# Kernel optimization log

Measured on AMD Instinct MI355X. Metric: run time of the kernel, lower is better.

Reference implementation:

```python
import jax, jax.numpy as jnp
import numpy as np

T, B, V, D, H, C = 2048, 32, 50257, 512, 768, 10


def setup_inputs() -> dict:
    key = jax.random.key(0)
    ks = jax.random.split(key, 11)
    s = 0.02
    return {
        "x": jax.random.randint(ks[0], (T, B), 0, V),
        "embed_table": jax.random.normal(ks[1], (V, D), jnp.float32) * s,
        "W_x": jax.random.normal(ks[2], (H, D), jnp.float32) * s,
        "W_f": jax.random.normal(ks[3], (H, D), jnp.float32) * s,
        "b_f": jax.random.normal(ks[4], (H,), jnp.float32) * s,
        "W_r": jax.random.normal(ks[5], (H, D), jnp.float32) * s,
        "b_r": jax.random.normal(ks[6], (H,), jnp.float32) * s,
        "W_cx": jax.random.normal(ks[7], (H, D), jnp.float32) * s,
        "b_cx": jax.random.normal(ks[8], (H,), jnp.float32) * s,
        "W_out": jax.random.normal(ks[9], (C, H), jnp.float32) * s,
        "b_out": jax.random.normal(ks[10], (C,), jnp.float32) * s,
    }


def reference(x, embed_table, W_x, W_f, b_f, W_r, b_r, W_cx, b_cx, W_out, b_out):
    # Embedding lookup: [T, B, D]
    e = embed_table[x]
    # Precompute all gate projections for every timestep (batched GEMMs).
    xp = jnp.einsum("tbd,hd->tbh", e, W_x)                 # x_t projection
    f = jax.nn.sigmoid(jnp.einsum("tbd,hd->tbh", e, W_f) + b_f)   # forget gate
    r = jax.nn.sigmoid(jnp.einsum("tbd,hd->tbh", e, W_r) + b_r)   # reset gate
    cx = jnp.einsum("tbd,hd->tbh", e, W_cx) + b_cx                # highway path

    c0 = jnp.zeros((B, H), e.dtype)  # init_hidden: zeros

    def step(c, inp):
        f_t, xp_t, r_t, cx_t = inp
        c = f_t * c + (1.0 - f_t) * xp_t
        h = r_t * jnp.tanh(c) + (1.0 - r_t) * cx_t
        return c, h

    _, ht = jax.lax.scan(step, c0, (f, xp, r, cx))  # ht: [T, B, H]

    # tanh -> max-pool over time -> tanh -> classifier
    pooled = jnp.max(jnp.tanh(ht), axis=0)          # [B, H]
    pooled = jnp.tanh(pooled)
    logit = pooled @ W_out.T + b_out                # [B, C]
    return logit
```

## Files before the change

kernel.cpp:

```cpp
#include <hip/hip_runtime.h>
#include <hip/hip_bf16.h>
#include <cstdint>
#include <cstddef>

#define T_DIM 2048
#define B_DIM 32
#define D_DIM 512
#define H_DIM 768
#define C_DIM 10
#define K_DIM D_DIM
#define N_DIM (4 * H_DIM)

#define TC 1024
#define NCHUNK (T_DIM / TC)
#define MC (TC * B_DIM)

#define L_SEG 64
#define S_SEG (TC / L_SEG)
#define BH (B_DIM * H_DIM)

typedef __attribute__((ext_vector_type(8))) short short8;
typedef __attribute__((ext_vector_type(4))) float float4v;

__device__ inline unsigned short f2bf(float f) {
  unsigned int u = __builtin_bit_cast(unsigned int, f);
  unsigned int r = (u + 0x7FFFu + ((u >> 16) & 1u)) >> 16;
  return (unsigned short)r;
}
__device__ inline float bf2f(unsigned short s) {
  unsigned int u = ((unsigned int)s) << 16;
  return __builtin_bit_cast(float, u);
}
__device__ inline float fast_rcp(float x) { return __builtin_amdgcn_rcpf(x); }
__device__ inline float fast_exp2(float x) { return __builtin_amdgcn_exp2f(x); }
__device__ inline float sigmoid_f(float x) {
  float e = fast_exp2(-1.4426950408889634f * x);
  return fast_rcp(1.0f + e);
}
__device__ inline float tanh_f(float x) {
  float e = fast_exp2(2.885390081777927f * x);
  return 1.0f - 2.0f * fast_rcp(e + 1.0f);
}
__device__ inline void gld16(const unsigned short* g, unsigned short* l) {
  __builtin_amdgcn_global_load_lds(
      (const __attribute__((address_space(1))) void*)g,
      (__attribute__((address_space(3))) void*)l, 16, 0, 0);
}
__device__ inline unsigned int pack_bf16x2(float lo, float hi) {
  return ((unsigned int)f2bf(hi) << 16) | (unsigned int)f2bf(lo);
}

__global__ __launch_bounds__(256) void gather_embed_kernel(
    const int* __restrict__ x_c, const float* __restrict__ table,
    unsigned short* __restrict__ ebfc) {
  int idx = blockIdx.x * 256 + threadIdx.x;
  int m = idx >> 7;
  int k4 = (idx & 127) << 2;
  int row = x_c[m];
  float4 v = *(const float4*)(table + (size_t)row * D_DIM + k4);
  ushort4 o;
  o.x = f2bf(v.x); o.y = f2bf(v.y); o.z = f2bf(v.z); o.w = f2bf(v.w);
  *(ushort4*)(ebfc + (size_t)m * D_DIM + k4) = o;
}

__global__ __launch_bounds__(256) void convert_w_kernel(
    const float* __restrict__ Wx, const float* __restrict__ Wf,
    const float* __restrict__ Wr, const float* __restrict__ Wcx,
    unsigned short* __restrict__ wcat) {
  int idx = blockIdx.x * 256 + threadIdx.x;
  int n = idx >> 7;
  int k4 = (idx & 127) << 2;
  int mat = n / H_DIM;
  int h = n - mat * H_DIM;
  const float* src = (mat == 0) ? Wx : (mat == 1) ? Wf : (mat == 2) ? Wr : Wcx;
  float4 v = *(const float4*)(src + (size_t)h * D_DIM + k4);
  ushort4 o;
  o.x = f2bf(v.x); o.y = f2bf(v.y); o.z = f2bf(v.z); o.w = f2bf(v.w);
  *(ushort4*)(wcat + (size_t)n * D_DIM + k4) = o;
}

#define BMT 256
#define BNT 256
#define BKT 64
#define NTILES (K_DIM / BKT)

__device__ __forceinline__ float4v mfma16(short8 a, short8 b, float4v c) {
  return __builtin_amdgcn_mfma_f32_16x16x32_bf16(a, b, c, 0, 0, 0);
}

__device__ __forceinline__ void stg(const unsigned short* src, unsigned short* sm,
                                    int pb, int isB, int h, int kt, int tid) {
  const unsigned short* s = src + (size_t)(h * 128) * K_DIM + kt * BKT;
  unsigned short* d = sm + pb * 32768 + isB * 16384 + h * 8192 + tid * 8;
  gld16(s, d);
  gld16(s + (size_t)64 * K_DIM, d + 4096);
}

template <int S1, int S2, int S3, int S4, int VMN>
__device__ __forceinline__ void tile_step(
    int u, unsigned short* sm, const unsigned short* srcA,
    const unsigned short* srcB, int tid, int aO, int bO, int c0, int c1,
    float4v (&acc)[8][4]) {
  const int pb = u & 1, pn = pb ^ 1;
  const int ab = pb * 32768 + aO;
  const int bb = pb * 32768 + bO;
  short8 a[4][2], b0[2][2], b1[2][2];

#pragma unroll
  for (int f = 0; f < 4; f++) {
    a[f][0] = *(const short8*)(sm + ab + f * 1024 + c0);
    a[f][1] = *(const short8*)(sm + ab + f * 1024 + c1);
  }
#pragma unroll
  for (int g = 0; g < 2; g++) {
    b0[g][0] = *(const short8*)(sm + bb + g * 1024 + c0);
    b0[g][1] = *(const short8*)(sm + bb + g * 1024 + c1);
  }
  if constexpr (S1) stg(srcA, sm, pn, 0, 0, u + 1, tid);
  __builtin_amdgcn_sched_barrier(0);
  __builtin_amdgcn_s_barrier();
  __builtin_amdgcn_s_setprio(1);
#pragma unroll
  for (int f = 0; f < 4; f++)
#pragma unroll
    for (int g = 0; g < 2; g++) {
      acc[f][g] = mfma16(a[f][0], b0[g][0], acc[f][g]);
      acc[f][g] = mfma16(a[f][1], b0[g][1], acc[f][g]);
    }
  __builtin_amdgcn_s_setprio(0);
  __builtin_amdgcn_sched_barrier(0);
  __builtin_amdgcn_s_barrier();

#pragma unroll
  for (int g = 0; g < 2; g++) {
    b1[g][0] = *(const short8*)(sm + bb + 2048 + g * 1024 + c0);
    b1[g][1] = *(const short8*)(sm + bb + 2048 + g * 1024 + c1);
  }
  if constexpr (S2) stg(srcA, sm, pn, 0, 1, u + 1, tid);
  __builtin_amdgcn_sched_barrier(0);
  __builtin_amdgcn_s_barrier();
  __builtin_amdgcn_s_setprio(1);
#pragma unroll
  for (int f = 0; f < 4; f++)
#pragma unroll
    for (int g = 0; g < 2; g++) {
      acc[f][2 + g] = mfma16(a[f][0], b1[g][0], acc[f][2 + g]);
      acc[f][2 + g] = mfma16(a[f][1], b1[g][1], acc[f][2 + g]);
    }
  __builtin_amdgcn_s_setprio(0);
  __builtin_amdgcn_sched_barrier(0);
  __builtin_amdgcn_s_barrier();

#pragma unroll
  for (int f = 0; f < 4; f++) {
    a[f][0] = *(const short8*)(sm + ab + 4096 + f * 1024 + c0);
    a[f][1] = *(const short8*)(sm + ab + 4096 + f * 1024 + c1);
  }
  if constexpr (S3) stg(srcB, sm, pb, 1, 0, u + 2, tid);
  __builtin_amdgcn_sched_barrier(0);
  __builtin_amdgcn_s_barrier();
  __builtin_amdgcn_s_setprio(1);
#pragma unroll
  for (int f = 0; f < 4; f++)
#pragma unroll
    for (int g = 0; g < 2; g++) {
      acc[4 + f][2 + g] = mfma16(a[f][0], b1[g][0], acc[4 + f][2 + g]);
      acc[4 + f][2 + g] = mfma16(a[f][1], b1[g][1], acc[4 + f][2 + g]);
    }
  __builtin_amdgcn_s_setprio(0);
  __builtin_amdgcn_sched_barrier(0);
  __builtin_amdgcn_s_barrier();

  if constexpr (S4) stg(srcB, sm, pb, 1, 1, u + 2, tid);
  __builtin_amdgcn_sched_barrier(0);
  __builtin_amdgcn_s_barrier();
  __builtin_amdgcn_s_setprio(1);
#pragma unroll
  for (int f = 0; f < 4; f++)
#pragma unroll
    for (int g = 0; g < 2; g++) {
      acc[4 + f][g] = mfma16(a[f][0], b0[g][0], acc[4 + f][g]);
      acc[4 + f][g] = mfma16(a[f][1], b0[g][1], acc[4 + f][g]);
    }
  __builtin_amdgcn_s_setprio(0);
  __builtin_amdgcn_sched_barrier(0);
  if constexpr (VMN == 4)
    asm volatile("s_waitcnt vmcnt(4)" ::: "memory");
  else if constexpr (VMN == 0)
    asm volatile("s_waitcnt vmcnt(0)" ::: "memory");
  __builtin_amdgcn_s_barrier();
}

__global__ __launch_bounds__(512, 2) void gemm_kernel(
    const unsigned short* __restrict__ ebfc,
    const unsigned short* __restrict__ wcat,
    const float* __restrict__ b_f, const float* __restrict__ b_r,
    const float* __restrict__ b_cx,
    unsigned short* __restrict__ projc) {
  __shared__ __align__(16) unsigned short smem[65536];

  const int tid = threadIdx.x;
  const int wave = tid >> 6;
  const int lane = tid & 63;
  const int quad = lane >> 4;
  const int l16 = lane & 15;
  const int wn = wave >> 2;
  const int wm = wave & 3;

  const int n0 = blockIdx.x * BNT;
  const int m0 = blockIdx.y * BMT;

  const int srow = tid >> 3;
  const int kch = (tid & 7) ^ (srow & 7);
  const unsigned short* srcA = wcat + (size_t)(n0 + srow) * K_DIM + kch * 8;
  const unsigned short* srcB = ebfc + (size_t)(m0 + srow) * K_DIM + kch * 8;

  const int aO = wn * 8192 + l16 * 64;
  const int bO = 16384 + (wm >> 1) * 8192 + (wm & 1) * 4096 + l16 * 64;
  const int c0 = (quad ^ (lane & 7)) * 8;
  const int c1 = ((quad ^ (lane & 7)) ^ 4) * 8;

  float4v acc[8][4] = {};

  stg(srcB, smem, 0, 1, 0, 0, tid);
  stg(srcB, smem, 0, 1, 1, 0, tid);
  stg(srcA, smem, 0, 0, 0, 0, tid);
  stg(srcA, smem, 0, 0, 1, 0, tid);
  stg(srcB, smem, 1, 1, 0, 1, tid);
  stg(srcB, smem, 1, 1, 1, 1, tid);
  asm volatile("s_waitcnt vmcnt(4)" ::: "memory");
  __builtin_amdgcn_s_barrier();

#pragma unroll 2
  for (int u = 0; u < NTILES - 2; u++)
    tile_step<1, 1, 1, 1, 4>(u, smem, srcA, srcB, tid, aO, bO, c0, c1, acc);
  tile_step<1, 1, 0, 0, 0>(NTILES - 2, smem, srcA, srcB, tid, aO, bO, c0, c1, acc);
  tile_step<0, 0, 0, 0, -1>(NTILES - 1, smem, srcA, srcB, tid, aO, bO, c0, c1, acc);

  int mat = n0 / H_DIM;
  int hb = n0 - mat * H_DIM;
  size_t matBase = (size_t)mat * MC * H_DIM;
  const float* bias = (mat == 1) ? b_f : (mat == 2) ? b_r : b_cx;
#pragma unroll
  for (int f = 0; f < 8; f++) {
    int hl = wn * 128 + f * 16 + quad * 4;
    float4 bv;
    if (mat == 0) { bv.x = bv.y = bv.z = bv.w = 0.0f; }
    else          { bv = *(const float4*)(bias + hb + hl); }
#pragma unroll
    for (int g = 0; g < 4; g++) {
      int ml = wm * 64 + g * 16 + l16;
      float v0 = acc[f][g][0] + bv.x;
      float v1 = acc[f][g][1] + bv.y;
      float v2 = acc[f][g][2] + bv.z;
      float v3 = acc[f][g][3] + bv.w;
      if (mat == 1 || mat == 2) {
        v0 = sigmoid_f(v0); v1 = sigmoid_f(v1);
        v2 = sigmoid_f(v2); v3 = sigmoid_f(v3);
      }
      uint2 pk;
      pk.x = pack_bf16x2(v0, v1);
      pk.y = pack_bf16x2(v2, v3);
      int log8 = hl >> 2;
      int phys8 = log8 ^ ((ml & 7) << 1);
      *(uint2*)(smem + ml * 256 + phys8 * 4) = pk;
    }
  }
  __syncthreads();
#pragma unroll
  for (int it = 0; it < 16; it++) {
    int idx = it * 512 + tid;
    int ml = idx >> 5;
    int c16 = idx & 31;
    int phys16 = c16 ^ (ml & 7);
    short8 v = *(const short8*)(smem + ml * 256 + phys16 * 8);
    *(short8*)(projc + matBase + (size_t)(m0 + ml) * H_DIM + hb + c16 * 8) = v;
  }
}

__global__ __launch_bounds__(128) void scan1_kernel(
    const unsigned short* __restrict__ projc,
    float* __restrict__ Pw, float* __restrict__ Qw) {
  int blk = blockIdx.x;
  int seg = blk / (BH / 512);
  int q   = blk % (BH / 512);
  int e4  = (q * 128 + threadIdx.x) * 4;
  const size_t mstr = (size_t)MC * H_DIM;
  size_t idx0 = (size_t)(seg * L_SEG) * BH + e4;
  float p0 = 1.f, p1 = 1.f, p2 = 1.f, p3 = 1.f;
  float c0 = 0.f, c1 = 0.f, c2 = 0.f, c3 = 0.f;
#pragma unroll 4
  for (int t = 0; t < L_SEG; t++) {
    size_t id = idx0 + (size_t)t * BH;
    ushort4 xp = *(const ushort4*)(projc + id);
    ushort4 ff = *(const ushort4*)(projc + mstr + id);
    float f0 = bf2f(ff.x), f1 = bf2f(ff.y), f2 = bf2f(ff.z), f3 = bf2f(ff.w);
    c0 = fmaf(f0, c0 - bf2f(xp.x), bf2f(xp.x));
    c1 = fmaf(f1, c1 - bf2f(xp.y), bf2f(xp.y));
    c2 = fmaf(f2, c2 - bf2f(xp.z), bf2f(xp.z));
    c3 = fmaf(f3, c3 - bf2f(xp.w), bf2f(xp.w));
    p0 *= f0; p1 *= f1; p2 *= f2; p3 *= f3;
  }
  int o = seg * BH + e4;
  *(float4*)(Pw + o) = make_float4(p0, p1, p2, p3);
  *(float4*)(Qw + o) = make_float4(c0, c1, c2, c3);
}

__global__ __launch_bounds__(256) void prefix_kernel(
    const float* __restrict__ Pw, const float* __restrict__ Qw,
    float* __restrict__ cin, float* __restrict__ c_state,
    const float* __restrict__ segmax, float* __restrict__ hm_state,
    int first, int hm_init) {
  int gid = blockIdx.x * 256 + threadIdx.x;
  float c = first ? 0.f : c_state[gid];
#pragma unroll
  for (int s = 0; s < S_SEG; s++) {
    cin[s * BH + gid] = c;
    c = fmaf(Pw[s * BH + gid], c, Qw[s * BH + gid]);
  }
  c_state[gid] = c;
  if (!first) {
    float m = segmax[gid];
#pragma unroll
    for (int s = 1; s < S_SEG; s++) m = fmaxf(m, segmax[s * BH + gid]);
    hm_state[gid] = hm_init ? m : fmaxf(hm_state[gid], m);
  }
}

__global__ __launch_bounds__(128) void scan2_kernel(
    const unsigned short* __restrict__ projc,
    const float* __restrict__ cin, float* __restrict__ segmax) {
  int blk = blockIdx.x;
  int seg = blk / (BH / 512);
  int q   = blk % (BH / 512);
  int e4  = (q * 128 + threadIdx.x) * 4;
  const size_t mstr = (size_t)MC * H_DIM;
  size_t idx0 = (size_t)(seg * L_SEG) * BH + e4;
  int o = seg * BH + e4;
  float4 cv = *(const float4*)(cin + o);
  float c0 = cv.x, c1 = cv.y, c2 = cv.z, c3 = cv.w;
  float m0 = -1e30f, m1 = -1e30f, m2 = -1e30f, m3 = -1e30f;
#pragma unroll 2
  for (int t = 0; t < L_SEG; t++) {
    size_t id = idx0 + (size_t)t * BH;
    ushort4 xp = *(const ushort4*)(projc + id);
    ushort4 ff = *(const ushort4*)(projc + mstr + id);
    ushort4 rr = *(const ushort4*)(projc + 2 * mstr + id);
    ushort4 cx = *(const ushort4*)(projc + 3 * mstr + id);
    c0 = fmaf(bf2f(ff.x), c0 - bf2f(xp.x), bf2f(xp.x));
    c1 = fmaf(bf2f(ff.y), c1 - bf2f(xp.y), bf2f(xp.y));
    c2 = fmaf(bf2f(ff.z), c2 - bf2f(xp.z), bf2f(xp.z));
    c3 = fmaf(bf2f(ff.w), c3 - bf2f(xp.w), bf2f(xp.w));
    float h0 = fmaf(bf2f(rr.x), tanh_f(c0) - bf2f(cx.x), bf2f(cx.x));
    float h1 = fmaf(bf2f(rr.y), tanh_f(c1) - bf2f(cx.y), bf2f(cx.y));
    float h2 = fmaf(bf2f(rr.z), tanh_f(c2) - bf2f(cx.z), bf2f(cx.z));
    float h3 = fmaf(bf2f(rr.w), tanh_f(c3) - bf2f(cx.w), bf2f(cx.w));
    m0 = fmaxf(m0, h0); m1 = fmaxf(m1, h1);
    m2 = fmaxf(m2, h2); m3 = fmaxf(m3, h3);
  }
  *(float4*)(segmax + o) = make_float4(m0, m1, m2, m3);
}

__global__ __launch_bounds__(256) void pool_final_kernel(
    const float* __restrict__ segmax, const float* __restrict__ hm_state,
    float* __restrict__ pooled) {
  int gid = blockIdx.x * 256 + threadIdx.x;
  float m = hm_state[gid];
#pragma unroll
  for (int s = 0; s < S_SEG; s++) m = fmaxf(m, segmax[s * BH + gid]);
  pooled[gid] = tanh_f(tanh_f(m));
}

__global__ __launch_bounds__(64) void classifier_kernel(
    const float* __restrict__ pooled, const float* __restrict__ W_out,
    const float* __restrict__ b_out, float* __restrict__ out) {
  int b = blockIdx.x / C_DIM;
  int c = blockIdx.x % C_DIM;
  int lane = threadIdx.x;
  float s = 0.0f;
#pragma unroll
  for (int i = 0; i < H_DIM / 64; i++) {
    int h = i * 64 + lane;
    s += pooled[(size_t)b * H_DIM + h] * W_out[(size_t)c * H_DIM + h];
  }
#pragma unroll
  for (int off = 32; off; off >>= 1) s += __shfl_down(s, off, 64);
  if (lane == 0) out[b * C_DIM + c] = s + b_out[c];
}

extern "C" void kernel_launch(void* const* d_in, const int* in_sizes, int n_in,
                              void* d_out, int out_size, void* d_ws, size_t ws_size,
                              hipStream_t stream) {
  const int*   x     = (const int*)d_in[0];
  const float* table = (const float*)d_in[1];
  const float* W_x   = (const float*)d_in[2];
  const float* W_f   = (const float*)d_in[3];
  const float* b_f   = (const float*)d_in[4];
  const float* W_r   = (const float*)d_in[5];
  const float* b_r   = (const float*)d_in[6];
  const float* W_cx  = (const float*)d_in[7];
  const float* b_cx  = (const float*)d_in[8];
  const float* W_out = (const float*)d_in[9];
  const float* b_out = (const float*)d_in[10];

  char* ws = (char*)d_ws;
  size_t off = 0;
  unsigned short* wcat  = (unsigned short*)(ws + off); off += (size_t)N_DIM * K_DIM * 2;
  unsigned short* ebfc  = (unsigned short*)(ws + off); off += (size_t)MC * K_DIM * 2;
  unsigned short* projc = (unsigned short*)(ws + off); off += (size_t)4 * MC * H_DIM * 2;
  float* Pw     = (float*)(ws + off); off += (size_t)S_SEG * BH * 4;
  float* Qw     = (float*)(ws + off); off += (size_t)S_SEG * BH * 4;
  float* cin    = (float*)(ws + off); off += (size_t)S_SEG * BH * 4;
  float* segmax = (float*)(ws + off); off += (size_t)S_SEG * BH * 4;
  float* c_st   = (float*)(ws + off); off += (size_t)BH * 4;
  float* hm_st  = (float*)(ws + off); off += (size_t)BH * 4;
  float* pooled = (float*)(ws + off); off += (size_t)BH * 4;

  convert_w_kernel<<<(N_DIM * K_DIM / 4) / 256, 256, 0, stream>>>(W_x, W_f, W_r, W_cx, wcat);

  dim3 g(N_DIM / BNT, MC / BMT);
  for (int ch = 0; ch < NCHUNK; ch++) {
    gather_embed_kernel<<<(MC * K_DIM / 4) / 256, 256, 0, stream>>>(x + (size_t)ch * MC, table, ebfc);
    gemm_kernel<<<g, 512, 0, stream>>>(ebfc, wcat, b_f, b_r, b_cx, projc);
    scan1_kernel<<<S_SEG * (BH / 512), 128, 0, stream>>>(projc, Pw, Qw);
    prefix_kernel<<<BH / 256, 256, 0, stream>>>(Pw, Qw, cin, c_st, segmax, hm_st,
                                                ch == 0, ch == 1);
    scan2_kernel<<<S_SEG * (BH / 512), 128, 0, stream>>>(projc, cin, segmax);
  }
  pool_final_kernel<<<BH / 256, 256, 0, stream>>>(segmax, hm_st, pooled);
  classifier_kernel<<<B_DIM * C_DIM, 64, 0, stream>>>(pooled, W_out, b_out, (float*)d_out);
}
```

Measured before the change: 553.8 us.

## Restructure GEMM to 128x256 tiles with triple-buffered BK=32 pipeline and XCD swizzle

Rewrites the projection GEMM to use 128x256 output tiles with a K-step of 32 and a three-slot shared-memory ring, prefetching two tiles ahead, in place of the 256x256, K=64 double-buffered scheme. Shared memory per block drops from 128 KB to 72 KB and launch bounds rise to 4 blocks per CU, aiming for higher occupancy and latency hiding. A 1D grid with a modulo-8 swizzle remaps blocks so that neighbouring tiles share operands within the same XCD's cache. The trade-offs are lower operand reuse per tile and more barriers per unit of work.

```diff
diff --git a/kernel.cpp b/kernel.cpp
--- a/kernel.cpp
+++ b/kernel.cpp
@@ -79,171 +79,125 @@
   *(ushort4*)(wcat + (size_t)n * D_DIM + k4) = o;
 }
 
-#define BMT 256
+#define BMT 128
 #define BNT 256
-#define BKT 64
-#define NTILES (K_DIM / BKT)
+#define BKT 32
+#define NT (K_DIM / BKT)
+#define BUF_SH 12288
 
 __device__ __forceinline__ float4v mfma16(short8 a, short8 b, float4v c) {
   return __builtin_amdgcn_mfma_f32_16x16x32_bf16(a, b, c, 0, 0, 0);
 }
 
-__device__ __forceinline__ void stg(const unsigned short* src, unsigned short* sm,
-                                    int pb, int isB, int h, int kt, int tid) {
-  const unsigned short* s = src + (size_t)(h * 128) * K_DIM + kt * BKT;
-  unsigned short* d = sm + pb * 32768 + isB * 16384 + h * 8192 + tid * 8;
+__device__ __forceinline__ void stgA(const unsigned short* srcA, unsigned short* sm,
+                                     int buf, int kt, int tid) {
+  const unsigned short* s = srcA + kt * BKT;
+  unsigned short* d = sm + buf * BUF_SH + tid * 8;
   gld16(s, d);
-  gld16(s + (size_t)64 * K_DIM, d + 4096);
-}
-
-template <int S1, int S2, int S3, int S4, int VMN>
+  gld16(s + (size_t)128 * K_DIM, d + 4096);
+}
+__device__ __forceinline__ void stgB(const unsigned short* srcB, unsigned short* sm,
+                                     int buf, int kt, int tid) {
+  gld16(srcB + kt * BKT, sm + buf * BUF_SH + 8192 + tid * 8);
+}
+
+template <int STG, int VMN>
 __device__ __forceinline__ void tile_step(
     int u, unsigned short* sm, const unsigned short* srcA,
-    const unsigned short* srcB, int tid, int aO, int bO, int c0, int c1,
-    float4v (&acc)[8][4]) {
-  const int pb = u & 1, pn = pb ^ 1;
-  const int ab = pb * 32768 + aO;
-  const int bb = pb * 32768 + bO;
-  short8 a[4][2], b0[2][2], b1[2][2];
-
-#pragma unroll
-  for (int f = 0; f < 4; f++) {
-    a[f][0] = *(const short8*)(sm + ab + f * 1024 + c0);
-    a[f][1] = *(const short8*)(sm + ab + f * 1024 + c1);
-  }
-#pragma unroll
-  for (int g = 0; g < 2; g++) {
-    b0[g][0] = *(const short8*)(sm + bb + g * 1024 + c0);
-    b0[g][1] = *(const short8*)(sm + bb + g * 1024 + c1);
-  }
-  if constexpr (S1) stg(srcA, sm, pn, 0, 0, u + 1, tid);
+    const unsigned short* srcB, int tid, int aO, int bO,
+    float4v (&acc)[4][4]) {
+  unsigned short* c = sm + (u % 3) * BUF_SH;
+  const int sbuf = (u + 2) % 3;
+  short8 a[4], b[4];
+#pragma unroll
+  for (int f = 0; f < 4; f++) a[f] = *(const short8*)(c + aO + f * 512);
+  b[0] = *(const short8*)(c + bO);
+  b[1] = *(const short8*)(c + bO + 512);
+  if constexpr (STG) stgA(srcA, sm, sbuf, u + 2, tid);
   __builtin_amdgcn_sched_barrier(0);
   __builtin_amdgcn_s_barrier();
   __builtin_amdgcn_s_setprio(1);
 #pragma unroll
-  for (int f = 0; f < 4; f++)
-#pragma unroll
-    for (int g = 0; g < 2; g++) {
-      acc[f][g] = mfma16(a[f][0], b0[g][0], acc[f][g]);
-      acc[f][g] = mfma16(a[f][1], b0[g][1], acc[f][g]);
-    }
+  for (int f = 0; f < 4; f++) {
+    acc[f][0] = mfma16(a[f], b[0], acc[f][0]);
+    acc[f][1] = mfma16(a[f], b[1], acc[f][1]);
+  }
   __builtin_amdgcn_s_setprio(0);
   __builtin_amdgcn_sched_barrier(0);
-  __builtin_amdgcn_s_barrier();
-
-#pragma unroll
-  for (int g = 0; g < 2; g++) {
-    b1[g][0] = *(const short8*)(sm + bb + 2048 + g * 1024 + c0);
-    b1[g][1] = *(const short8*)(sm + bb + 2048 + g * 1024 + c1);
-  }
-  if constexpr (S2) stg(srcA, sm, pn, 0, 1, u + 1, tid);
+  b[2] = *(const short8*)(c + bO + 1024);
+  b[3] = *(const short8*)(c + bO + 1536);
+  if constexpr (STG) stgB(srcB, sm, sbuf, u + 2, tid);
   __builtin_amdgcn_sched_barrier(0);
-  __builtin_amdgcn_s_barrier();
   __builtin_amdgcn_s_setprio(1);
 #pragma unroll
-  for (int f = 0; f < 4; f++)
-#pragma unroll
-    for (int g = 0; g < 2; g++) {
-      acc[f][2 + g] = mfma16(a[f][0], b1[g][0], acc[f][2 + g]);
-      acc[f][2 + g] = mfma16(a[f][1], b1[g][1], acc[f][2 + g]);
-    }
+  for (int f = 0; f < 4; f++) {
+    acc[f][2] = mfma16(a[f], b[2], acc[f][2]);
+    acc[f][3] = mfma16(a[f], b[3], acc[f][3]);
+  }
   __builtin_amdgcn_s_setprio(0);
   __builtin_amdgcn_sched_barrier(0);
-  __builtin_amdgcn_s_barrier();
-
-#pragma unroll
-  for (int f = 0; f < 4; f++) {
-    a[f][0] = *(const short8*)(sm + ab + 4096 + f * 1024 + c0);
-    a[f][1] = *(const short8*)(sm + ab + 4096 + f * 1024 + c1);
-  }
-  if constexpr (S3) stg(srcB, sm, pb, 1, 0, u + 2, tid);
-  __builtin_amdgcn_sched_barrier(0);
-  __builtin_amdgcn_s_barrier();
-  __builtin_amdgcn_s_setprio(1);
-#pragma unroll
-  for (int f = 0; f < 4; f++)
-#pragma unroll
-    for (int g = 0; g < 2; g++) {
-      acc[4 + f][2 + g] = mfma16(a[f][0], b1[g][0], acc[4 + f][2 + g]);
-      acc[4 + f][2 + g] = mfma16(a[f][1], b1[g][1], acc[4 + f][2 + g]);
-    }
-  __builtin_amdgcn_s_setprio(0);
-  __builtin_amdgcn_sched_barrier(0);
-  __builtin_amdgcn_s_barrier();
-
-  if constexpr (S4) stg(srcB, sm, pb, 1, 1, u + 2, tid);
-  __builtin_amdgcn_sched_barrier(0);
-  __builtin_amdgcn_s_barrier();
-  __builtin_amdgcn_s_setprio(1);
-#pragma unroll
-  for (int f = 0; f < 4; f++)
-#pragma unroll
-    for (int g = 0; g < 2; g++) {
-      acc[4 + f][g] = mfma16(a[f][0], b0[g][0], acc[4 + f][g]);
-      acc[4 + f][g] = mfma16(a[f][1], b0[g][1], acc[4 + f][g]);
-    }
-  __builtin_amdgcn_s_setprio(0);
-  __builtin_amdgcn_sched_barrier(0);
-  if constexpr (VMN == 4)
-    asm volatile("s_waitcnt vmcnt(4)" ::: "memory");
+  if constexpr (VMN == 3)
+    asm volatile("s_waitcnt vmcnt(3)" ::: "memory");
   else if constexpr (VMN == 0)
     asm volatile("s_waitcnt vmcnt(0)" ::: "memory");
   __builtin_amdgcn_s_barrier();
 }
 
-__global__ __launch_bounds__(512, 2) void gemm_kernel(
+__global__ __launch_bounds__(512, 4) void gemm_kernel(
     const unsigned short* __restrict__ ebfc,
     const unsigned short* __restrict__ wcat,
     const float* __restrict__ b_f, const float* __restrict__ b_r,
     const float* __restrict__ b_cx,
     unsigned short* __restrict__ projc) {
-  __shared__ __align__(16) unsigned short smem[65536];
+  __shared__ __align__(16) unsigned short smem[36864];
 
   const int tid = threadIdx.x;
   const int wave = tid >> 6;
   const int lane = tid & 63;
   const int quad = lane >> 4;
   const int l16 = lane & 15;
-  const int wn = wave >> 2;
-  const int wm = wave & 3;
-
-  const int n0 = blockIdx.x * BNT;
-  const int m0 = blockIdx.y * BMT;
-
-  const int srow = tid >> 3;
-  const int kch = (tid & 7) ^ (srow & 7);
-  const unsigned short* srcA = wcat + (size_t)(n0 + srow) * K_DIM + kch * 8;
-  const unsigned short* srcB = ebfc + (size_t)(m0 + srow) * K_DIM + kch * 8;
-
-  const int aO = wn * 8192 + l16 * 64;
-  const int bO = 16384 + (wm >> 1) * 8192 + (wm & 1) * 4096 + l16 * 64;
-  const int c0 = (quad ^ (lane & 7)) * 8;
-  const int c1 = ((quad ^ (lane & 7)) ^ 4) * 8;
-
-  float4v acc[8][4] = {};
-
-  stg(srcB, smem, 0, 1, 0, 0, tid);
-  stg(srcB, smem, 0, 1, 1, 0, tid);
-  stg(srcA, smem, 0, 0, 0, 0, tid);
-  stg(srcA, smem, 0, 0, 1, 0, tid);
-  stg(srcB, smem, 1, 1, 0, 1, tid);
-  stg(srcB, smem, 1, 1, 1, 1, tid);
-  asm volatile("s_waitcnt vmcnt(4)" ::: "memory");
+  const int wn = wave >> 1;
+  const int wm = wave & 1;
+
+  const int orig = blockIdx.x;
+  const int swz = (orig & 7) * 384 + (orig >> 3);
+  const int n_idx = swz % 12;
+  const int m_idx = swz / 12;
+  const int n0 = n_idx * BNT;
+  const int m0 = m_idx * BMT;
+
+  const int arow = tid >> 2;
+  const int kchx = (tid & 3) ^ (arow & 3);
+  const unsigned short* srcA = wcat + (size_t)(n0 + arow) * K_DIM + kchx * 8;
+  const unsigned short* srcB = ebfc + (size_t)(m0 + arow) * K_DIM + kchx * 8;
+
+  const int xr = (quad ^ (l16 & 3)) * 8;
+  const int aO = (wn * 64 + l16) * 32 + xr;
+  const int bO = 8192 + (wm * 64 + l16) * 32 + xr;
+
+  float4v acc[4][4] = {};
+
+  stgA(srcA, smem, 0, 0, tid);
+  stgB(srcB, smem, 0, 0, tid);
+  stgA(srcA, smem, 1, 1, tid);
+  stgB(srcB, smem, 1, 1, tid);
+  asm volatile("s_waitcnt vmcnt(3)" ::: "memory");
   __builtin_amdgcn_s_barrier();
 
-#pragma unroll 2
-  for (int u = 0; u < NTILES - 2; u++)
-    tile_step<1, 1, 1, 1, 4>(u, smem, srcA, srcB, tid, aO, bO, c0, c1, acc);
-  tile_step<1, 1, 0, 0, 0>(NTILES - 2, smem, srcA, srcB, tid, aO, bO, c0, c1, acc);
-  tile_step<0, 0, 0, 0, -1>(NTILES - 1, smem, srcA, srcB, tid, aO, bO, c0, c1, acc);
-
+#pragma unroll
+  for (int u = 0; u < NT - 2; u++)
+    tile_step<1, 3>(u, smem, srcA, srcB, tid, aO, bO, acc);
+  tile_step<0, 0>(NT - 2, smem, srcA, srcB, tid, aO, bO, acc);
+  tile_step<0, -1>(NT - 1, smem, srcA, srcB, tid, aO, bO, acc);
+
+  __syncthreads();
   int mat = n0 / H_DIM;
   int hb = n0 - mat * H_DIM;
   size_t matBase = (size_t)mat * MC * H_DIM;
   const float* bias = (mat == 1) ? b_f : (mat == 2) ? b_r : b_cx;
 #pragma unroll
-  for (int f = 0; f < 8; f++) {
-    int hl = wn * 128 + f * 16 + quad * 4;
+  for (int f = 0; f < 4; f++) {
+    int hl = wn * 64 + f * 16 + quad * 4;
     float4 bv;
     if (mat == 0) { bv.x = bv.y = bv.z = bv.w = 0.0f; }
     else          { bv = *(const float4*)(bias + hb + hl); }
@@ -268,7 +222,7 @@
   }
   __syncthreads();
 #pragma unroll
-  for (int it = 0; it < 16; it++) {
+  for (int it = 0; it < 8; it++) {
     int idx = it * 512 + tid;
     int ml = idx >> 5;
     int c16 = idx & 31;
@@ -418,10 +372,9 @@
 
   convert_w_kernel<<<(N_DIM * K_DIM / 4) / 256, 256, 0, stream>>>(W_x, W_f, W_r, W_cx, wcat);
 
-  dim3 g(N_DIM / BNT, MC / BMT);
   for (int ch = 0; ch < NCHUNK; ch++) {
     gather_embed_kernel<<<(MC * K_DIM / 4) / 256, 256, 0, stream>>>(x + (size_t)ch * MC, table, ebfc);
-    gemm_kernel<<<g, 512, 0, stream>>>(ebfc, wcat, b_f, b_r, b_cx, projc);
+    gemm_kernel<<<(N_DIM / BNT) * (MC / BMT), 512, 0, stream>>>(ebfc, wcat, b_f, b_r, b_cx, projc);
     scan1_kernel<<<S_SEG * (BH / 512), 128, 0, stream>>>(projc, Pw, Qw);
     prefix_kernel<<<BH / 256, 256, 0, stream>>>(Pw, Qw, cin, c_st, segmax, hm_st,
                                                 ch == 0, ch == 1);
```

Measured after the change: 523.5 us. -5.5%, faster.
